# Optimization experiments

Measured on AMD Instinct MI355X. Metric: run time of the kernel, lower is better.

## Reference

```python
import jax, jax.numpy as jnp
import numpy as np

B = 2048
T = 720
V = 64
K = 4
PHI_MAX = 0.25
N_KNOTS = 4


def setup_inputs() -> dict:
    key = jax.random.key(0)
    k1, k2, k3, k4 = jax.random.split(key, 4)
    y_hat = jax.random.normal(k1, (B, T, V), dtype=jnp.float32)
    # learned params (perturbed from the zero/one init so the edit is non-trivial)
    a = 0.1 * jax.random.normal(k2, (V, K), dtype=jnp.float32)
    phi = 0.1 * jax.random.normal(k3, (V, K), dtype=jnp.float32)
    env_knots = jax.random.uniform(k4, (V, N_KNOTS), dtype=jnp.float32, minval=0.5, maxval=1.5)
    k_bins = jnp.array([4, 30, 60, 120], dtype=jnp.int32)  # rFFT bin indices, < T//2+1
    return {"y_hat": y_hat, "a": a, "phi": phi, "env_knots": env_knots, "k_bins": k_bins}


def reference(y_hat, a, phi, env_knots, k_bins):
    Bn, Tn, Vn = y_hat.shape
    # full rFFT along time: [B, F, V] complex, F = T//2 + 1
    Fspec = jnp.fft.rfft(y_hat, n=Tn, axis=1)
    # per-(variable, bin) complex gain: (1 + a) * exp(i * tanh(phi) * phi_max)
    amp = 1.0 + a                               # [V, K]
    ph = jnp.tanh(phi) * PHI_MAX                # [V, K]
    scale = (amp * jnp.exp(1j * ph)).T          # [K, V] complex
    # edit only the seasonal bins (vectorized equivalent of the nested loops)
    Fspec = Fspec.at[:, k_bins, :].multiply(scale[None, :, :])
    y_corr = jnp.fft.irfft(Fspec, n=Tn, axis=1)  # [B, T, V] real
    # piecewise-linear envelope over [0, 1] with N_KNOTS control points
    t = jnp.linspace(0.0, 1.0, Tn)               # [T]
    pos = t * (N_KNOTS - 1)
    idx = jnp.clip(pos.astype(jnp.int32), 0, N_KNOTS - 2)  # [T]
    frac = pos - idx.astype(t.dtype)
    knots = jnp.clip(env_knots, 0.5, 1.5)        # [V, n_knots]
    env = knots[:, idx] * (1.0 - frac) + knots[:, idx + 1] * frac  # [V, T]
    return y_corr * env.T[None, :, :]
```

## Files before the change

kernel.cpp:

```cpp
#include <hip/hip_runtime.h>
#include <hip/hip_fp16.h>
#include <math.h>

#define T_LEN   720
#define V_DIM   64
#define KBINS   4
#define NKNOTS  4
#define BLOCK   768
#define TSLICE  15
#define NW      12
#define PIPE    5
#define YLS     33

#define WS_TABH 0
#define WS_SR   2880
#define WS_SI   3136
#define WS_KN   3392

__device__ __forceinline__ unsigned f2bf_rne(float f) {
    unsigned u = __float_as_uint(f);
    return (u + 0x7FFFu + ((u >> 16) & 1u)) >> 16;
}
__device__ __forceinline__ float bf2f(unsigned h) {
    return __uint_as_float(h << 16);
}

__global__ __launch_bounds__(256) void precompute_kernel(
    const float* __restrict__ a, const float* __restrict__ phi,
    const float* __restrict__ env_knots, const int* __restrict__ k_bins,
    float* __restrict__ ws)
{
    int id = blockIdx.x * 256 + threadIdx.x;
    if (id < T_LEN) {
        int t = id;
        __half h[8];
        #pragma unroll
        for (int k = 0; k < 4; ++k) {
            int kb = k_bins[k];
            int m  = (kb * t) % T_LEN;
            float th = (float)m * 0.00872664625997164788f;
            float sn, cs;
            sincosf(th, &sn, &cs);
            h[k]     = __float2half_rn(cs);
            h[4 + k] = __float2half_rn(sn);
        }
        ((uint4*)(ws + WS_TABH))[t] = *(const uint4*)(&h[0]);
    } else if (id < T_LEN + V_DIM * KBINS) {
        int e = id - T_LEN;
        int v = e >> 2, k = e & 3;
        float amp = 1.0f + a[e];
        float ph  = tanhf(phi[e]) * 0.25f;
        float sp, cp;
        sincosf(ph, &sp, &cp);
        ws[WS_SR + k * V_DIM + v] = amp * cp - 1.0f;
        ws[WS_SI + k * V_DIM + v] = amp * sp;
    } else if (id < T_LEN + V_DIM * KBINS + V_DIM * NKNOTS) {
        int e = id - T_LEN - V_DIM * KBINS;
        int v = e >> 2, n = e & 3;
        ws[WS_KN + n * V_DIM + v] = fminf(fmaxf(env_knots[e], 0.5f), 1.5f);
    }
}

__global__ __launch_bounds__(BLOCK) void SeasonalEnvelopeAdapter_kernel(
    const float* __restrict__ y,
    const float* __restrict__ ws,
    float* __restrict__ out)
{
    __shared__ __align__(16) __half tabh[T_LEN][8];
    __shared__ unsigned int yldsU[T_LEN * YLS];
    __shared__ float red[16][NW][33];
    __shared__ __align__(16) float coefT[8][V_DIM];

    const int tid  = threadIdx.x;
    const int b    = blockIdx.x;
    const int g    = tid & 15;
    const int s    = tid >> 4;
    const int lane = tid & 63;
    const int w    = tid >> 6;

    if (tid < T_LEN)
        *(uint4*)(&tabh[tid][0]) = ((const uint4*)(ws + WS_TABH))[tid];
    __syncthreads();

    const size_t base = (size_t)b * (T_LEN * V_DIM) + (size_t)(g << 2);
    float accre[4][4], accim[4][4];
    #pragma unroll
    for (int j = 0; j < 4; ++j)
        #pragma unroll
        for (int k = 0; k < 4; ++k) { accre[j][k] = 0.f; accim[j][k] = 0.f; }

    {
        float4 yv[PIPE];
        #pragma unroll
        for (int i0 = 0; i0 < PIPE; ++i0)
            yv[i0] = *(const float4*)(y + base + (size_t)(48 * i0 + s) * V_DIM);
        #pragma unroll
        for (int i = 0; i < TSLICE; ++i) {
            int t = 48 * i + s;
            float4 cur = yv[i % PIPE];
            if (i + PIPE < TSLICE)
                yv[i % PIPE] = *(const float4*)(y + base + (size_t)(48 * (i + PIPE) + s) * V_DIM);
            yldsU[t * YLS + (g << 1)]     = f2bf_rne(cur.x) | (f2bf_rne(cur.y) << 16);
            yldsU[t * YLS + (g << 1) + 1] = f2bf_rne(cur.z) | (f2bf_rne(cur.w) << 16);
            uint4 hp = *(const uint4*)(&tabh[t][0]);
            const __half* h = (const __half*)&hp;
            const float cs[4] = {__half2float(h[0]), __half2float(h[1]),
                                 __half2float(h[2]), __half2float(h[3])};
            const float sn[4] = {__half2float(h[4]), __half2float(h[5]),
                                 __half2float(h[6]), __half2float(h[7])};
            const float yj[4] = {cur.x, cur.y, cur.z, cur.w};
            #pragma unroll
            for (int j = 0; j < 4; ++j)
                #pragma unroll
                for (int k = 0; k < 4; ++k) {
                    accre[j][k] = fmaf(yj[j], cs[k], accre[j][k]);
                    accim[j][k] = fmaf(yj[j], sn[k], accim[j][k]);
                }
        }
    }

    #pragma unroll
    for (int j = 0; j < 4; ++j)
        #pragma unroll
        for (int k = 0; k < 4; ++k) {
            float r = accre[j][k], im = accim[j][k];
            r  += __shfl_xor(r, 16, 64);  r  += __shfl_xor(r, 32, 64);
            im += __shfl_xor(im, 16, 64); im += __shfl_xor(im, 32, 64);
            accre[j][k] = r; accim[j][k] = im;
        }
    if (lane < 16) {
        #pragma unroll
        for (int j = 0; j < 4; ++j)
            #pragma unroll
            for (int k = 0; k < 4; ++k) {
                red[lane][w][j * 8 + k]     = accre[j][k];
                red[lane][w][j * 8 + 4 + k] = accim[j][k];
            }
    }
    __syncthreads();

    if (tid < 256) {
        int v = tid >> 2, k = tid & 3;
        int gg = v >> 2, j = v & 3;
        float cr = 0.f, ci = 0.f;
        #pragma unroll
        for (int ww = 0; ww < NW; ++ww) {
            cr += red[gg][ww][j * 8 + k];
            ci += red[gg][ww][j * 8 + 4 + k];
        }
        float sr = ws[WS_SR + k * V_DIM + v];
        float si = ws[WS_SI + k * V_DIM + v];
        const float sc = 2.0f / (float)T_LEN;
        coefT[k][v]     = (cr * sr + ci * si) * sc;
        coefT[4 + k][v] = (cr * si - ci * sr) * sc;
    }
    __syncthreads();

    float cre[4][4], cim[4][4];
    #pragma unroll
    for (int k = 0; k < 4; ++k) {
        float4 r4 = *(const float4*)(&coefT[k][g << 2]);
        float4 i4 = *(const float4*)(&coefT[4 + k][g << 2]);
        cre[k][0] = r4.x; cre[k][1] = r4.y; cre[k][2] = r4.z; cre[k][3] = r4.w;
        cim[k][0] = i4.x; cim[k][1] = i4.y; cim[k][2] = i4.z; cim[k][3] = i4.w;
    }
    float kn0[4], kn1[4], kn2[4], kn3[4];
    {
        float4 a4 = *(const float4*)(ws + WS_KN + 0 * V_DIM + (g << 2));
        float4 b4 = *(const float4*)(ws + WS_KN + 1 * V_DIM + (g << 2));
        float4 c4 = *(const float4*)(ws + WS_KN + 2 * V_DIM + (g << 2));
        float4 d4 = *(const float4*)(ws + WS_KN + 3 * V_DIM + (g << 2));
        kn0[0]=a4.x; kn0[1]=a4.y; kn0[2]=a4.z; kn0[3]=a4.w;
        kn1[0]=b4.x; kn1[1]=b4.y; kn1[2]=b4.z; kn1[3]=b4.w;
        kn2[0]=c4.x; kn2[1]=c4.y; kn2[2]=c4.z; kn2[3]=c4.w;
        kn3[0]=d4.x; kn3[1]=d4.y; kn3[2]=d4.z; kn3[3]=d4.w;
    }

    const float posScale = 3.0f / 719.0f;
    #pragma unroll
    for (int i = 0; i < TSLICE; ++i) {
        int t = 48 * i + s;
        unsigned p0 = yldsU[t * YLS + (g << 1)];
        unsigned p1 = yldsU[t * YLS + (g << 1) + 1];
        const float yj[4] = { bf2f(p0 & 0xFFFFu), bf2f(p0 >> 16),
                              bf2f(p1 & 0xFFFFu), bf2f(p1 >> 16) };
        uint4 hp = *(const uint4*)(&tabh[t][0]);
        const __half* h = (const __half*)&hp;
        const float cs[4] = {__half2float(h[0]), __half2float(h[1]),
                             __half2float(h[2]), __half2float(h[3])};
        const float sn[4] = {__half2float(h[4]), __half2float(h[5]),
                             __half2float(h[6]), __half2float(h[7])};
        float pos = (float)t * posScale;
        int idx = (int)pos; idx = idx > 2 ? 2 : idx;
        float frac = pos - (float)idx;
        float oj[4];
        #pragma unroll
        for (int j = 0; j < 4; ++j) {
            float d = 0.f;
            #pragma unroll
            for (int k = 0; k < 4; ++k)
                d = fmaf(cre[k][j], cs[k], fmaf(-cim[k][j], sn[k], d));
            float e0 = (idx == 0) ? kn0[j] : ((idx == 1) ? kn1[j] : kn2[j]);
            float e1 = (idx == 0) ? kn1[j] : ((idx == 1) ? kn2[j] : kn3[j]);
            float env = fmaf(e1 - e0, frac, e0);
            oj[j] = (yj[j] + d) * env;
        }
        float4 o; o.x = oj[0]; o.y = oj[1]; o.z = oj[2]; o.w = oj[3];
        *(float4*)(out + base + (size_t)t * V_DIM) = o;
    }
}

extern "C" void kernel_launch(void* const* d_in, const int* in_sizes, int n_in,
                              void* d_out, int out_size, void* d_ws, size_t ws_size,
                              hipStream_t stream) {
    const float* y         = (const float*)d_in[0];
    const float* a         = (const float*)d_in[1];
    const float* phi       = (const float*)d_in[2];
    const float* env_knots = (const float*)d_in[3];
    const int*   k_bins    = (const int*)d_in[4];
    float* out = (float*)d_out;
    float* ws  = (float*)d_ws;

    int B = in_sizes[0] / (T_LEN * V_DIM);
    int ids = T_LEN + V_DIM * KBINS + V_DIM * NKNOTS;
    precompute_kernel<<<(ids + 255) / 256, 256, 0, stream>>>(a, phi, env_knots, k_bins, ws);
    SeasonalEnvelopeAdapter_kernel<<<B, BLOCK, 0, stream>>>(y, ws, out);
}
```

Baseline: 180.2 us.

## Split fused kernel into coefficient and apply passes, dropping LDS staging of y

The single fused kernel is replaced by two kernels. The first computes the per-batch seasonal-bin coefficients and stashes them in the output buffer as scratch. The second reloads y from global memory, applies the correction and envelope, and visits batches in reverse order so recently read data may still be cached. This removes the roughly 95KB bf16 LDS staging of y and the bf16 rounding, and moves to 256-thread blocks for higher occupancy. The cost is reading y from HBM twice in a purely bandwidth-bound workload, plus an extra kernel launch.

```diff
diff --git a/kernel.cpp b/kernel.cpp
--- a/kernel.cpp
+++ b/kernel.cpp
@@ -6,24 +6,15 @@
 #define V_DIM   64
 #define KBINS   4
 #define NKNOTS  4
-#define BLOCK   768
-#define TSLICE  15
-#define NW      12
-#define PIPE    5
-#define YLS     33
+#define BLOCK   256
+#define TSLICE  45
+#define NW      4
+#define PIPE    4
 
 #define WS_TABH 0
 #define WS_SR   2880
 #define WS_SI   3136
 #define WS_KN   3392
-
-__device__ __forceinline__ unsigned f2bf_rne(float f) {
-    unsigned u = __float_as_uint(f);
-    return (u + 0x7FFFu + ((u >> 16) & 1u)) >> 16;
-}
-__device__ __forceinline__ float bf2f(unsigned h) {
-    return __uint_as_float(h << 16);
-}
 
 __global__ __launch_bounds__(256) void precompute_kernel(
     const float* __restrict__ a, const float* __restrict__ phi,
@@ -61,15 +52,13 @@
     }
 }
 
-__global__ __launch_bounds__(BLOCK) void SeasonalEnvelopeAdapter_kernel(
+__global__ __launch_bounds__(BLOCK) void coef_kernel(
     const float* __restrict__ y,
     const float* __restrict__ ws,
-    float* __restrict__ out)
+    float* __restrict__ coefOut)
 {
-    __shared__ __align__(16) __half tabh[T_LEN][8];
-    __shared__ unsigned int yldsU[T_LEN * YLS];
+    __shared__ __align__(16) uint4 tabh[T_LEN];
     __shared__ float red[16][NW][33];
-    __shared__ __align__(16) float coefT[8][V_DIM];
 
     const int tid  = threadIdx.x;
     const int b    = blockIdx.x;
@@ -78,8 +67,8 @@
     const int lane = tid & 63;
     const int w    = tid >> 6;
 
-    if (tid < T_LEN)
-        *(uint4*)(&tabh[tid][0]) = ((const uint4*)(ws + WS_TABH))[tid];
+    for (int e = tid; e < T_LEN; e += BLOCK)
+        tabh[e] = ((const uint4*)(ws + WS_TABH))[e];
     __syncthreads();
 
     const size_t base = (size_t)b * (T_LEN * V_DIM) + (size_t)(g << 2);
@@ -89,34 +78,30 @@
         #pragma unroll
         for (int k = 0; k < 4; ++k) { accre[j][k] = 0.f; accim[j][k] = 0.f; }
 
-    {
-        float4 yv[PIPE];
-        #pragma unroll
-        for (int i0 = 0; i0 < PIPE; ++i0)
-            yv[i0] = *(const float4*)(y + base + (size_t)(48 * i0 + s) * V_DIM);
-        #pragma unroll
-        for (int i = 0; i < TSLICE; ++i) {
-            int t = 48 * i + s;
-            float4 cur = yv[i % PIPE];
-            if (i + PIPE < TSLICE)
-                yv[i % PIPE] = *(const float4*)(y + base + (size_t)(48 * (i + PIPE) + s) * V_DIM);
-            yldsU[t * YLS + (g << 1)]     = f2bf_rne(cur.x) | (f2bf_rne(cur.y) << 16);
-            yldsU[t * YLS + (g << 1) + 1] = f2bf_rne(cur.z) | (f2bf_rne(cur.w) << 16);
-            uint4 hp = *(const uint4*)(&tabh[t][0]);
-            const __half* h = (const __half*)&hp;
-            const float cs[4] = {__half2float(h[0]), __half2float(h[1]),
-                                 __half2float(h[2]), __half2float(h[3])};
-            const float sn[4] = {__half2float(h[4]), __half2float(h[5]),
-                                 __half2float(h[6]), __half2float(h[7])};
-            const float yj[4] = {cur.x, cur.y, cur.z, cur.w};
+    float4 yv[PIPE];
+    #pragma unroll
+    for (int i0 = 0; i0 < PIPE; ++i0)
+        yv[i0] = *(const float4*)(y + base + (size_t)(16 * i0 + s) * V_DIM);
+    #pragma unroll
+    for (int i = 0; i < TSLICE; ++i) {
+        const int t = 16 * i + s;
+        float4 cur = yv[i & 3];
+        if (i + PIPE < TSLICE)
+            yv[i & 3] = *(const float4*)(y + base + (size_t)(16 * (i + PIPE) + s) * V_DIM);
+        uint4 hp = tabh[t];
+        const __half* h = (const __half*)&hp;
+        const float cs[4] = {__half2float(h[0]), __half2float(h[1]),
+                             __half2float(h[2]), __half2float(h[3])};
+        const float sn[4] = {__half2float(h[4]), __half2float(h[5]),
+                             __half2float(h[6]), __half2float(h[7])};
+        const float yj[4] = {cur.x, cur.y, cur.z, cur.w};
+        #pragma unroll
+        for (int j = 0; j < 4; ++j)
             #pragma unroll
-            for (int j = 0; j < 4; ++j)
-                #pragma unroll
-                for (int k = 0; k < 4; ++k) {
-                    accre[j][k] = fmaf(yj[j], cs[k], accre[j][k]);
-                    accim[j][k] = fmaf(yj[j], sn[k], accim[j][k]);
-                }
-        }
+            for (int k = 0; k < 4; ++k) {
+                accre[j][k] = fmaf(yj[j], cs[k], accre[j][k]);
+                accim[j][k] = fmaf(yj[j], sn[k], accim[j][k]);
+            }
     }
 
     #pragma unroll
@@ -138,53 +123,72 @@
             }
     }
     __syncthreads();
-
-    if (tid < 256) {
-        int v = tid >> 2, k = tid & 3;
-        int gg = v >> 2, j = v & 3;
+    {
+        const int e = tid;
+        const int k = e >> 6, v = e & 63;
+        const int gg = v >> 2, j = v & 3;
         float cr = 0.f, ci = 0.f;
         #pragma unroll
         for (int ww = 0; ww < NW; ++ww) {
             cr += red[gg][ww][j * 8 + k];
             ci += red[gg][ww][j * 8 + 4 + k];
         }
-        float sr = ws[WS_SR + k * V_DIM + v];
-        float si = ws[WS_SI + k * V_DIM + v];
+        float sr = ws[WS_SR + e];
+        float si = ws[WS_SI + e];
         const float sc = 2.0f / (float)T_LEN;
-        coefT[k][v]     = (cr * sr + ci * si) * sc;
-        coefT[4 + k][v] = (cr * si - ci * sr) * sc;
-    }
-    __syncthreads();
-
+        float* cb = coefOut + (size_t)b * (T_LEN * V_DIM);
+        cb[e]       = (cr * sr + ci * si) * sc;
+        cb[256 + e] = (cr * si - ci * sr) * sc;
+    }
+}
+
+__global__ __launch_bounds__(BLOCK) void apply_kernel(
+    const float* __restrict__ y,
+    const float* __restrict__ ws,
+    float* __restrict__ out,
+    int B)
+{
+    __shared__ __align__(16) uint4 tabh[T_LEN];
+
+    const int tid = threadIdx.x;
+    const int b   = B - 1 - blockIdx.x;
+    const int g   = tid & 15;
+    const int s   = tid >> 4;
+
+    for (int e = tid; e < T_LEN; e += BLOCK)
+        tabh[e] = ((const uint4*)(ws + WS_TABH))[e];
+
+    const float* cb = out + (size_t)b * (T_LEN * V_DIM);
     float cre[4][4], cim[4][4];
     #pragma unroll
     for (int k = 0; k < 4; ++k) {
-        float4 r4 = *(const float4*)(&coefT[k][g << 2]);
-        float4 i4 = *(const float4*)(&coefT[4 + k][g << 2]);
+        float4 r4 = *(const float4*)(cb + k * 64 + (g << 2));
+        float4 i4 = *(const float4*)(cb + 256 + k * 64 + (g << 2));
         cre[k][0] = r4.x; cre[k][1] = r4.y; cre[k][2] = r4.z; cre[k][3] = r4.w;
         cim[k][0] = i4.x; cim[k][1] = i4.y; cim[k][2] = i4.z; cim[k][3] = i4.w;
     }
-    float kn0[4], kn1[4], kn2[4], kn3[4];
-    {
-        float4 a4 = *(const float4*)(ws + WS_KN + 0 * V_DIM + (g << 2));
-        float4 b4 = *(const float4*)(ws + WS_KN + 1 * V_DIM + (g << 2));
-        float4 c4 = *(const float4*)(ws + WS_KN + 2 * V_DIM + (g << 2));
-        float4 d4 = *(const float4*)(ws + WS_KN + 3 * V_DIM + (g << 2));
-        kn0[0]=a4.x; kn0[1]=a4.y; kn0[2]=a4.z; kn0[3]=a4.w;
-        kn1[0]=b4.x; kn1[1]=b4.y; kn1[2]=b4.z; kn1[3]=b4.w;
-        kn2[0]=c4.x; kn2[1]=c4.y; kn2[2]=c4.z; kn2[3]=c4.w;
-        kn3[0]=d4.x; kn3[1]=d4.y; kn3[2]=d4.z; kn3[3]=d4.w;
-    }
-
+    float kn[4][4];
+    #pragma unroll
+    for (int n = 0; n < 4; ++n) {
+        float4 k4 = *(const float4*)(ws + WS_KN + n * V_DIM + (g << 2));
+        kn[n][0] = k4.x; kn[n][1] = k4.y; kn[n][2] = k4.z; kn[n][3] = k4.w;
+    }
+    __syncthreads();
+
+    const size_t base = (size_t)b * (T_LEN * V_DIM) + (size_t)(g << 2);
     const float posScale = 3.0f / 719.0f;
+
+    float4 zv[PIPE];
+    #pragma unroll
+    for (int i0 = 0; i0 < PIPE; ++i0)
+        zv[i0] = *(const float4*)(y + base + (size_t)(16 * i0 + s) * V_DIM);
     #pragma unroll
     for (int i = 0; i < TSLICE; ++i) {
-        int t = 48 * i + s;
-        unsigned p0 = yldsU[t * YLS + (g << 1)];
-        unsigned p1 = yldsU[t * YLS + (g << 1) + 1];
-        const float yj[4] = { bf2f(p0 & 0xFFFFu), bf2f(p0 >> 16),
-                              bf2f(p1 & 0xFFFFu), bf2f(p1 >> 16) };
-        uint4 hp = *(const uint4*)(&tabh[t][0]);
+        const int t = 16 * i + s;
+        float4 cur = zv[i & 3];
+        if (i + PIPE < TSLICE)
+            zv[i & 3] = *(const float4*)(y + base + (size_t)(16 * (i + PIPE) + s) * V_DIM);
+        uint4 hp = tabh[t];
         const __half* h = (const __half*)&hp;
         const float cs[4] = {__half2float(h[0]), __half2float(h[1]),
                              __half2float(h[2]), __half2float(h[3])};
@@ -193,19 +197,19 @@
         float pos = (float)t * posScale;
         int idx = (int)pos; idx = idx > 2 ? 2 : idx;
         float frac = pos - (float)idx;
-        float oj[4];
+        const float yj[4] = {cur.x, cur.y, cur.z, cur.w};
+        float4 o;
         #pragma unroll
         for (int j = 0; j < 4; ++j) {
             float d = 0.f;
             #pragma unroll
             for (int k = 0; k < 4; ++k)
                 d = fmaf(cre[k][j], cs[k], fmaf(-cim[k][j], sn[k], d));
-            float e0 = (idx == 0) ? kn0[j] : ((idx == 1) ? kn1[j] : kn2[j]);
-            float e1 = (idx == 0) ? kn1[j] : ((idx == 1) ? kn2[j] : kn3[j]);
+            float e0 = (idx == 0) ? kn[0][j] : ((idx == 1) ? kn[1][j] : kn[2][j]);
+            float e1 = (idx == 0) ? kn[1][j] : ((idx == 1) ? kn[2][j] : kn[3][j]);
             float env = fmaf(e1 - e0, frac, e0);
-            oj[j] = (yj[j] + d) * env;
-        }
-        float4 o; o.x = oj[0]; o.y = oj[1]; o.z = oj[2]; o.w = oj[3];
+            ((float*)&o)[j] = (yj[j] + d) * env;
+        }
         *(float4*)(out + base + (size_t)t * V_DIM) = o;
     }
 }
@@ -224,5 +228,6 @@
     int B = in_sizes[0] / (T_LEN * V_DIM);
     int ids = T_LEN + V_DIM * KBINS + V_DIM * NKNOTS;
     precompute_kernel<<<(ids + 255) / 256, 256, 0, stream>>>(a, phi, env_knots, k_bins, ws);
-    SeasonalEnvelopeAdapter_kernel<<<B, BLOCK, 0, stream>>>(y, ws, out);
-}
+    coef_kernel<<<B, BLOCK, 0, stream>>>(y, ws, out);
+    apply_kernel<<<B, BLOCK, 0, stream>>>(y, ws, out, B);
+}
```

Result: slower. 228.3 us (+26.7%).
